# Kernel tuning notes

Hardware: AMD Instinct MI355X
Metric: run time of the kernel (lower is better)

Reference implementation:

```python
import jax, jax.numpy as jnp
import numpy as np

EPS = 1e-8

def _gelu(x):
    return jax.nn.gelu(x, approximate=False)  # torch F.gelu default (erf)

def _film_pool(feat, q, film_w, film_b, hid_w, hid_b, fin_w, fin_b):
    # feat: (B,C,H,W), q: (B,Q,E)
    B, C, H, W = feat.shape
    f = feat.reshape(B, C, H * W).transpose(0, 2, 1)            # (B,HW,C)
    gb = q @ film_w + film_b                                    # (B,Q,2C)
    gamma, beta = jnp.split(gb, 2, axis=-1)                     # (B,Q,C) each
    mod = gamma[:, :, None, :] * f[:, None, :, :] + beta[:, :, None, :]  # (B,Q,HW,C)
    h = _gelu(mod @ hid_w + hid_b)                              # (B,Q,HW,Hh)
    attn = jax.nn.sigmoid(h @ fin_w + fin_b)                    # (B,Q,HW,1)
    pooled = (attn * mod).sum(axis=2) / (attn.sum(axis=2) + EPS)  # (B,Q,C)
    return pooled, attn[..., 0]                                 # attn map (B,Q,HW)

def setup_inputs() -> dict:
    key = jax.random.key(0)
    ks = jax.random.split(key, 32)
    B, Q, E, Hh = 2, 32, 768, 128
    chans = [64, 128, 256]
    hws = [(80, 80), (40, 40), (20, 20)]
    d = {}
    d['feat0'] = jax.random.normal(ks[0], (B, chans[0], *hws[0]), jnp.float32)
    d['feat1'] = jax.random.normal(ks[1], (B, chans[1], *hws[1]), jnp.float32)
    d['feat2'] = jax.random.normal(ks[2], (B, chans[2], *hws[2]), jnp.float32)
    d['fact_embeddings'] = jax.random.normal(ks[3], (B, Q, E), jnp.float32)
    for i, C in enumerate(chans):
        d[f'film_w{i}'] = jax.random.normal(ks[4 + 4 * i], (E, 2 * C), jnp.float32) * 0.02
        d[f'film_b{i}'] = jnp.zeros((2 * C,), jnp.float32)
        d[f'hid_w{i}'] = jax.random.normal(ks[5 + 4 * i], (C, Hh), jnp.float32) * 0.05
        d[f'hid_b{i}'] = jnp.zeros((Hh,), jnp.float32)
        d[f'fin_w{i}'] = jax.random.normal(ks[6 + 4 * i], (Hh, 1), jnp.float32) * 0.05
        d[f'fin_b{i}'] = jnp.zeros((1,), jnp.float32)
    in_dim = sum(chans) + hws[-1][0] * hws[-1][1]  # 448 + 400 = 848
    d['mlp_w1'] = jax.random.normal(ks[20], (in_dim, 512), jnp.float32) * 0.02
    d['mlp_b1'] = jnp.zeros((512,), jnp.float32)
    d['mlp_w2'] = jax.random.normal(ks[21], (512, 256), jnp.float32) * 0.02
    d['mlp_b2'] = jnp.zeros((256,), jnp.float32)
    d['mlp_w3'] = jax.random.normal(ks[22], (256, 1), jnp.float32) * 0.02
    d['mlp_b3'] = jnp.zeros((1,), jnp.float32)
    return d

def reference(feat0, feat1, feat2, fact_embeddings,
              film_w0, film_b0, hid_w0, hid_b0, fin_w0, fin_b0,
              film_w1, film_b1, hid_w1, hid_b1, fin_w1, fin_b1,
              film_w2, film_b2, hid_w2, hid_b2, fin_w2, fin_b2,
              mlp_w1, mlp_b1, mlp_w2, mlp_b2, mlp_w3, mlp_b3):
    q = fact_embeddings
    p0, _ = _film_pool(feat0, q, film_w0, film_b0, hid_w0, hid_b0, fin_w0, fin_b0)
    p1, _ = _film_pool(feat1, q, film_w1, film_b1, hid_w1, hid_b1, fin_w1, fin_b1)
    p2, a2 = _film_pool(feat2, q, film_w2, film_b2, hid_w2, hid_b2, fin_w2, fin_b2)
    cat = jnp.concatenate([p0, p1, p2, a2], axis=2)  # (B,Q,848)
    x = _gelu(cat @ mlp_w1 + mlp_b1)
    x = _gelu(x @ mlp_w2 + mlp_b2)
    logits = (x @ mlp_w3 + mlp_b3)[..., 0]  # (B,Q)
    return logits
```

## Files before the change

kernel.cpp:

```cpp
#include <hip/hip_runtime.h>
#include <math.h>

#define BQ 64
#define HH 128
#define EPS 1e-8f

typedef short bf16x8 __attribute__((ext_vector_type(8)));
typedef float f32x4  __attribute__((ext_vector_type(4)));

__device__ __forceinline__ float gelu_exact(float x) {
    return 0.5f * x * (1.0f + erff(x * 0.70710678118654752440f));
}

__device__ __forceinline__ unsigned bf16_rne(float x) {
    unsigned u = __float_as_uint(x);
    return (u + 0x7FFFu + ((u >> 16) & 1u)) >> 16;
}
__device__ __forceinline__ uint2 split_pack(float a, float b) {
    unsigned ha = bf16_rne(a);
    float fa = __uint_as_float(ha << 16);
    unsigned la = bf16_rne(a - fa);
    unsigned hb = bf16_rne(b);
    float fb = __uint_as_float(hb << 16);
    unsigned lb = bf16_rne(b - fb);
    uint2 r; r.x = ha | (hb << 16); r.y = la | (lb << 16);
    return r;
}

__device__ __forceinline__
void pack_feat_body(int i,
                    const float* __restrict__ f0, const float* __restrict__ f1,
                    const float* __restrict__ f2,
                    unsigned short* __restrict__ p0h, unsigned short* __restrict__ p0l,
                    unsigned short* __restrict__ p1h, unsigned short* __restrict__ p1l,
                    unsigned short* __restrict__ p2h, unsigned short* __restrict__ p2l)
{
    const float* f; unsigned short *oh, *ol; int HW; int idx;
    if (i < 102400)      { f = f0; oh = p0h; ol = p0l; HW = 6400; idx = i; }
    else if (i < 153600) { f = f1; oh = p1h; ol = p1l; HW = 1600; idx = i - 102400; }
    else if (i < 179200) { f = f2; oh = p2h; ol = p2l; HW = 400;  idx = i - 153600; }
    else return;
    const int px = idx % HW;
    const int cgb = idx / HW;
    const float* src = f + ((size_t)cgb * 8) * HW + px;
    float a[8];
    #pragma unroll
    for (int k = 0; k < 8; ++k) a[k] = src[(size_t)k * HW];
    unsigned hwd[4], lwd[4];
    #pragma unroll
    for (int k = 0; k < 4; ++k) {
        uint2 p = split_pack(a[2 * k], a[2 * k + 1]);
        hwd[k] = p.x; lwd[k] = p.y;
    }
    *(uint4*)&oh[(size_t)idx * 8] = make_uint4(hwd[0], hwd[1], hwd[2], hwd[3]);
    *(uint4*)&ol[(size_t)idx * 8] = make_uint4(lwd[0], lwd[1], lwd[2], lwd[3]);
}

__global__ __launch_bounds__(256)
void prep1_kernel(const float* __restrict__ f0, const float* __restrict__ f1,
                  const float* __restrict__ f2,
                  unsigned short* __restrict__ p0h, unsigned short* __restrict__ p0l,
                  unsigned short* __restrict__ p1h, unsigned short* __restrict__ p1l,
                  unsigned short* __restrict__ p2h, unsigned short* __restrict__ p2l,
                  const float* __restrict__ qe,
                  const float* __restrict__ fw0, const float* __restrict__ fb0,
                  const float* __restrict__ fw1, const float* __restrict__ fb1,
                  const float* __restrict__ fw2, const float* __restrict__ fb2,
                  float* __restrict__ gb0, float* __restrict__ gb1, float* __restrict__ gb2)
{
    const int tid = threadIdx.x;
    if (blockIdx.x < 700) {
        pack_feat_body(blockIdx.x * 256 + tid, f0, f1, f2, p0h, p0l, p1h, p1l, p2h, p2l);
        return;
    }
    __shared__ float sq[768];
    __shared__ float sP[256];
    const int bb = blockIdx.x - 700;
    const int chunk = bb >> 6, bq = bb & 63;
    int s, o0;
    if (chunk == 0)      { s = 0; o0 = 0; }
    else if (chunk <= 2) { s = 1; o0 = (chunk - 1) * 128; }
    else                 { s = 2; o0 = (chunk - 3) * 128; }
    const float* fw  = s == 0 ? fw0 : s == 1 ? fw1 : fw2;
    const float* fbv = s == 0 ? fb0 : s == 1 ? fb1 : fb2;
    float* gb        = s == 0 ? gb0 : s == 1 ? gb1 : gb2;
    const int twoC = 128 << s;

    for (int i = tid; i < 768; i += 256) sq[i] = qe[bq * 768 + i];
    __syncthreads();
    const int o = o0 + (tid & 127), half = tid >> 7;
    const int e0 = half * 384;
    float a0 = 0.f, a1 = 0.f;
    #pragma unroll 2
    for (int e = 0; e < 384; e += 2) {
        a0 = fmaf(sq[e0 + e],     fw[(e0 + e) * twoC + o],     a0);
        a1 = fmaf(sq[e0 + e + 1], fw[(e0 + e + 1) * twoC + o], a1);
    }
    sP[tid] = a0 + a1;
    __syncthreads();
    if (tid < 128) {
        int oo = o0 + tid;
        gb[bq * twoC + oo] = sP[tid] + sP[tid + 128] + fbv[oo];
    }
}

__global__ __launch_bounds__(256)
void prep2_kernel(const float* __restrict__ gb0, const float* __restrict__ gb1,
                  const float* __restrict__ gb2,
                  const float* __restrict__ hw0_, const float* __restrict__ hb0,
                  const float* __restrict__ hw1_, const float* __restrict__ hb1,
                  const float* __restrict__ hw2_, const float* __restrict__ hb2,
                  unsigned short* __restrict__ g0h, unsigned short* __restrict__ g0l,
                  unsigned short* __restrict__ g1h, unsigned short* __restrict__ g1l,
                  unsigned short* __restrict__ g2h, unsigned short* __restrict__ g2l,
                  float* __restrict__ b20, float* __restrict__ b21, float* __restrict__ b22)
{
    const int tid = threadIdx.x;
    if (blockIdx.x < 1792) {
        int i = blockIdx.x * 256 + tid;
        const float *gb, *hw; unsigned short *oh, *ol; int C, idx;
        if (i < 65536)       { gb = gb0; hw = hw0_; oh = g0h; ol = g0l; C = 64;  idx = i; }
        else if (i < 196608) { gb = gb1; hw = hw1_; oh = g1h; ol = g1l; C = 128; idx = i - 65536; }
        else                 { gb = gb2; hw = hw2_; oh = g2h; ol = g2l; C = 256; idx = i - 196608; }
        const int j  = idx & 127;
        const int cg = (idx >> 7) % (C / 8);
        const int bq = idx / (128 * (C / 8));
        const int c0 = cg * 8;
        const float* g = gb + bq * 2 * C;
        float a[8];
        #pragma unroll
        for (int k = 0; k < 8; ++k) a[k] = g[c0 + k] * hw[(size_t)(c0 + k) * HH + j];
        unsigned hwd[4], lwd[4];
        #pragma unroll
        for (int k = 0; k < 4; ++k) {
            uint2 p = split_pack(a[2 * k], a[2 * k + 1]);
            hwd[k] = p.x; lwd[k] = p.y;
        }
        *(uint4*)&oh[(size_t)idx * 8] = make_uint4(hwd[0], hwd[1], hwd[2], hwd[3]);
        *(uint4*)&ol[(size_t)idx * 8] = make_uint4(lwd[0], lwd[1], lwd[2], lwd[3]);
        return;
    }
    __shared__ float sBeta[256];
    __shared__ float sP[256];
    const int bb = blockIdx.x - 1792;
    const int s = bb >> 6, bq = bb & 63;
    const float* gb = s == 0 ? gb0 : s == 1 ? gb1 : gb2;
    const float* hw = s == 0 ? hw0_ : s == 1 ? hw1_ : hw2_;
    const float* hb = s == 0 ? hb0 : s == 1 ? hb1 : hb2;
    float* b2       = s == 0 ? b20 : s == 1 ? b21 : b22;
    const int C = 64 << s;

    for (int i = tid; i < C; i += 256) sBeta[i] = gb[bq * 2 * C + C + i];
    __syncthreads();
    const int j = tid & 127, half = tid >> 7;
    const int c0 = half * (C / 2);
    float acc = 0.f;
    for (int c = 0; c < C / 2; ++c)
        acc = fmaf(sBeta[c0 + c], hw[(c0 + c) * HH + j], acc);
    sP[tid] = acc;
    __syncthreads();
    if (tid < 128) b2[bq * HH + tid] = hb[tid] + sP[tid] + sP[tid + 128];
}

#define MFMA3(ACC, ALO, AHI, BH, BL)                                            \
    ACC = __builtin_amdgcn_mfma_f32_16x16x32_bf16(ALO, BH, ACC, 0, 0, 0);       \
    ACC = __builtin_amdgcn_mfma_f32_16x16x32_bf16(AHI, BL, ACC, 0, 0, 0);       \
    ACC = __builtin_amdgcn_mfma_f32_16x16x32_bf16(AHI, BH, ACC, 0, 0, 0);

template<int C, bool WRITE_ATTN>
__device__ __forceinline__
void pool_body(const float* __restrict__ feat, int HW,
               const unsigned short* __restrict__ fh, const unsigned short* __restrict__ fl,
               const unsigned short* __restrict__ gwh, const unsigned short* __restrict__ gwl,
               const float* __restrict__ b2, const float* __restrict__ finw,
               const float* __restrict__ finb,
               float* __restrict__ Sout, float* __restrict__ attn_out,
               int b, int qp, int tile,
               unsigned short* sB, float* sAttn)
{
    const int tid  = threadIdx.x;
    const int w    = tid >> 6;
    const int lane = tid & 63;
    const int l15  = lane & 15, l4 = lane >> 4;
    const int px0  = tile * 256;
    constexpr int CG = C / 8;
    const int bq0 = b * 32 + qp * 2;
    const int bq1 = bq0 + 1;
    const float* fbase = feat + (size_t)b * C * HW;

    f32x4 accA[2][8], accB[2][8];
    #pragma unroll
    for (int jt = 0; jt < 8; ++jt) {
        float bv0 = b2[bq0 * HH + jt * 16 + l15];
        float bv1 = b2[bq1 * HH + jt * 16 + l15];
        accA[0][jt] = (f32x4){bv0, bv0, bv0, bv0};
        accA[1][jt] = (f32x4){bv0, bv0, bv0, bv0};
        accB[0][jt] = (f32x4){bv1, bv1, bv1, bv1};
        accB[1][jt] = (f32x4){bv1, bv1, bv1, bv1};
    }

    const int apx0 = min(px0 + (w * 2 + 0) * 16 + l15, HW - 1);
    const int apx1 = min(px0 + (w * 2 + 1) * 16 + l15, HW - 1);
    const unsigned short* fhp = fh + (size_t)b * CG * HW * 8;
    const unsigned short* flp = fl + (size_t)b * CG * HW * 8;
    const unsigned short* q0h = gwh + (size_t)bq0 * CG * 1024;
    const unsigned short* q0l = gwl + (size_t)bq0 * CG * 1024;
    const unsigned short* q1h = gwh + (size_t)bq1 * CG * 1024;
    const unsigned short* q1l = gwl + (size_t)bq1 * CG * 1024;

    for (int ks = 0; ks < CG / 4; ++ks) {
        const size_t arow = (size_t)(ks * 4 + l4) * HW;
        const bf16x8 Ahi0 = *(const bf16x8*)(fhp + (arow + apx0) * 8);
        const bf16x8 Alo0 = *(const bf16x8*)(flp + (arow + apx0) * 8);
        const bf16x8 Ahi1 = *(const bf16x8*)(fhp + (arow + apx1) * 8);
        const bf16x8 Alo1 = *(const bf16x8*)(flp + (arow + apx1) * 8);
        {
            uint4* dst = (uint4*)sB;
            dst[tid]        = ((const uint4*)(q0h + (size_t)ks * 4096))[tid];
            dst[512  + tid] = ((const uint4*)(q0l + (size_t)ks * 4096))[tid];
            dst[1024 + tid] = ((const uint4*)(q1h + (size_t)ks * 4096))[tid];
            dst[1536 + tid] = ((const uint4*)(q1l + (size_t)ks * 4096))[tid];
        }
        __syncthreads();
        const int bofs = (l4 * 128 + l15) * 8;
        #pragma unroll
        for (int jt = 0; jt < 8; ++jt) {
            const bf16x8 B0h = *(const bf16x8*)(sB + bofs + jt * 128);
            const bf16x8 B0l = *(const bf16x8*)(sB + 4096 + bofs + jt * 128);
            MFMA3(accA[0][jt], Alo0, Ahi0, B0h, B0l)
            MFMA3(accA[1][jt], Alo1, Ahi1, B0h, B0l)
            const bf16x8 B1h = *(const bf16x8*)(sB + 8192 + bofs + jt * 128);
            const bf16x8 B1l = *(const bf16x8*)(sB + 12288 + bofs + jt * 128);
            MFMA3(accB[0][jt], Alo0, Ahi0, B1h, B1l)
            MFMA3(accB[1][jt], Alo1, Ahi1, B1h, B1l)
        }
        __syncthreads();
    }

    const float fb0 = finb[0];
    #pragma unroll
    for (int pt = 0; pt < 2; ++pt) {
        float p0[4] = {0.f, 0.f, 0.f, 0.f};
        float p1[4] = {0.f, 0.f, 0.f, 0.f};
        #pragma unroll
        for (int jt = 0; jt < 8; ++jt) {
            float fwv = finw[jt * 16 + l15];
            #pragma unroll
            for (int r = 0; r < 4; ++r) {
                p0[r] = fmaf(gelu_exact(accA[pt][jt][r]), fwv, p0[r]);
                p1[r] = fmaf(gelu_exact(accB[pt][jt][r]), fwv, p1[r]);
            }
        }
        #pragma unroll
        for (int r = 0; r < 4; ++r) {
            p0[r] += __shfl_xor(p0[r], 1);  p1[r] += __shfl_xor(p1[r], 1);
            p0[r] += __shfl_xor(p0[r], 2);  p1[r] += __shfl_xor(p1[r], 2);
            p0[r] += __shfl_xor(p0[r], 4);  p1[r] += __shfl_xor(p1[r], 4);
            p0[r] += __shfl_xor(p0[r], 8);  p1[r] += __shfl_xor(p1[r], 8);
        }
        if (l15 == 0) {
            #pragma unroll
            for (int r = 0; r < 4; ++r) {
                int lpx = (w * 2 + pt) * 16 + l4 * 4 + r;
                int px  = px0 + lpx;
                float a0v = (px < HW) ? 1.0f / (1.0f + expf(-(p0[r] + fb0))) : 0.0f;
                float a1v = (px < HW) ? 1.0f / (1.0f + expf(-(p1[r] + fb0))) : 0.0f;
                sAttn[lpx]       = a0v;
                sAttn[256 + lpx] = a1v;
                if (WRITE_ATTN && px < HW) {
                    attn_out[bq0 * HW + px] = a0v;
                    attn_out[bq1 * HW + px] = a1v;
                }
            }
        }
    }
    __syncthreads();

    {
        float sa = sAttn[tid];
        #pragma unroll
        for (int d = 1; d < 64; d <<= 1) sa += __shfl_xor(sa, d);
        if (lane == 0) {
            int bqx = (tid < 256) ? bq0 : bq1;
            atomicAdd(&Sout[bqx * (C + 1) + C], sa);
        }
    }

    constexpr int CPW = C / 8;
    #pragma unroll 1
    for (int ci = 0; ci < CPW; ++ci) {
        const int c2 = w * CPW + ci;
        const float* fr = fbase + (size_t)c2 * HW;
        float s0 = 0.f, s1 = 0.f;
        #pragma unroll
        for (int k = 0; k < 4; ++k) {
            int lpx = lane + 64 * k;
            int gc = min(px0 + lpx, HW - 1);
            float fv = fr[gc];
            s0 = fmaf(fv, sAttn[lpx], s0);
            s1 = fmaf(fv, sAttn[256 + lpx], s1);
        }
        #pragma unroll
        for (int d = 1; d < 64; d <<= 1) {
            s0 += __shfl_xor(s0, d);
            s1 += __shfl_xor(s1, d);
        }
        if (lane == 0) {
            atomicAdd(&Sout[bq0 * (C + 1) + c2], s0);
            atomicAdd(&Sout[bq1 * (C + 1) + c2], s1);
        }
    }
}

__global__ __launch_bounds__(512)
void pool_fused(const unsigned short* __restrict__ f0h, const unsigned short* __restrict__ f0l,
                const unsigned short* __restrict__ f1h, const unsigned short* __restrict__ f1l,
                const unsigned short* __restrict__ f2h, const unsigned short* __restrict__ f2l,
                const unsigned short* __restrict__ g0h, const unsigned short* __restrict__ g0l,
                const unsigned short* __restrict__ g1h, const unsigned short* __restrict__ g1l,
                const unsigned short* __restrict__ g2h, const unsigned short* __restrict__ g2l,
                const float* __restrict__ feat0, const float* __restrict__ feat1,
                const float* __restrict__ feat2,
                const float* __restrict__ b20, const float* __restrict__ b21,
                const float* __restrict__ b22,
                const float* __restrict__ finw0, const float* __restrict__ finb0,
                const float* __restrict__ finw1, const float* __restrict__ finb1,
                const float* __restrict__ finw2, const float* __restrict__ finb2,
                float* __restrict__ S0, float* __restrict__ S1, float* __restrict__ S2,
                float* __restrict__ attn2)
{
    __shared__ __align__(16) unsigned short sB[16384];
    __shared__ float sAttn[512];
    const int blk = blockIdx.x;
    if (blk < 64) {
        int bt = blk >> 4, qp = blk & 15;
        int b = bt >> 1, t = bt & 1;
        pool_body<256, true>(feat2, 400, f2h, f2l, g2h, g2l, b22, finw2, finb2,
                             S2, attn2, b, qp, t, sB, sAttn);
    } else if (blk < 288) {
        int bb = blk - 64; int bt = bb >> 4, qp = bb & 15;
        int b = bt / 7, t = bt % 7;
        pool_body<128, false>(feat1, 1600, f1h, f1l, g1h, g1l, b21, finw1, finb1,
                              S1, nullptr, b, qp, t, sB, sAttn);
    } else {
        int bb = blk - 288; int bt = bb >> 4, qp = bb & 15;
        int b = bt / 25, t = bt % 25;
        pool_body<64, false>(feat0, 6400, f0h, f0l, g0h, g0l, b20, finw0, finb0,
                             S0, nullptr, b, qp, t, sB, sAttn);
    }
}

__global__ __launch_bounds__(256)
void mlp1_kernel(const float* __restrict__ S0, const float* __restrict__ S1,
                 const float* __restrict__ S2,
                 const float* __restrict__ gb0, const float* __restrict__ gb1,
                 const float* __restrict__ gb2,
                 const float* __restrict__ attn2,
                 const float* __restrict__ w1, const float* __restrict__ b1,
                 float* __restrict__ X1)
{
    __shared__ float sCat[848];
    __shared__ float sP[256];
    const int tid = threadIdx.x, bq = blockIdx.x;

    for (int i = tid; i < 448; i += 256) {
        int sc, c;
        if (i < 64)       { sc = 0; c = i; }
        else if (i < 192) { sc = 1; c = i - 64; }
        else              { sc = 2; c = i - 192; }
        const int C = 64 << sc;
        const float* So = (sc == 0) ? S0 : (sc == 1) ? S1 : S2;
        const float* g  = (sc == 0) ? gb0 : (sc == 1) ? gb1 : gb2;
        float Sa = So[bq * (C + 1) + C];
        float Sf = So[bq * (C + 1) + c];
        float gamma = g[bq * 2 * C + c];
        float beta  = g[bq * 2 * C + C + c];
        sCat[i] = (gamma * Sf + beta * Sa) / (Sa + EPS);
    }
    for (int i = tid; i < 400; i += 256) sCat[448 + i] = attn2[bq * 400 + i];
    __syncthreads();

    const int o = blockIdx.y * 128 + (tid & 127), half = tid >> 7;
    const int k0 = half * 424;
    float a0 = 0.f, a1 = 0.f;
    #pragma unroll 2
    for (int k = 0; k < 424; k += 2) {
        a0 = fmaf(sCat[k0 + k],     w1[(k0 + k) * 512 + o],     a0);
        a1 = fmaf(sCat[k0 + k + 1], w1[(k0 + k + 1) * 512 + o], a1);
    }
    sP[tid] = a0 + a1;
    __syncthreads();
    if (tid < 128) {
        int oo = blockIdx.y * 128 + tid;
        X1[bq * 512 + oo] = sP[tid] + sP[tid + 128] + b1[oo];
    }
}

__global__ __launch_bounds__(256)
void mlp23_kernel(const float* __restrict__ X1,
                  const float* __restrict__ w2, const float* __restrict__ b2,
                  const float* __restrict__ w3, const float* __restrict__ b3,
                  float* __restrict__ out)
{
    __shared__ float sX1[512];
    __shared__ float sX2[256];
    __shared__ float sR[4];
    const int tid = threadIdx.x, bq = blockIdx.x;
    for (int i = tid; i < 512; i += 256) sX1[i] = gelu_exact(X1[bq * 512 + i]);
    __syncthreads();
    float a0 = b2[tid], a1 = 0.f, a2 = 0.f, a3 = 0.f;
    #pragma unroll 4
    for (int k = 0; k < 512; k += 4) {
        a0 = fmaf(sX1[k],     w2[(k)     * 256 + tid], a0);
        a1 = fmaf(sX1[k + 1], w2[(k + 1) * 256 + tid], a1);
        a2 = fmaf(sX1[k + 2], w2[(k + 2) * 256 + tid], a2);
        a3 = fmaf(sX1[k + 3], w2[(k + 3) * 256 + tid], a3);
    }
    sX2[tid] = gelu_exact((a0 + a1) + (a2 + a3));
    __syncthreads();
    float p = sX2[tid] * w3[tid];
    #pragma unroll
    for (int d = 1; d < 64; d <<= 1) p += __shfl_xor(p, d);
    if ((tid & 63) == 0) sR[tid >> 6] = p;
    __syncthreads();
    if (tid == 0) out[bq] = sR[0] + sR[1] + sR[2] + sR[3] + b3[0];
}

extern "C" void kernel_launch(void* const* d_in, const int* in_sizes, int n_in,
                              void* d_out, int out_size, void* d_ws, size_t ws_size,
                              hipStream_t stream)
{
    const float* feat0 = (const float*)d_in[0];
    const float* feat1 = (const float*)d_in[1];
    const float* feat2 = (const float*)d_in[2];
    const float* qe    = (const float*)d_in[3];
    const float* film_w0 = (const float*)d_in[4];
    const float* film_b0 = (const float*)d_in[5];
    const float* hid_w0  = (const float*)d_in[6];
    const float* hid_b0  = (const float*)d_in[7];
    const float* fin_w0  = (const float*)d_in[8];
    const float* fin_b0  = (const float*)d_in[9];
    const float* film_w1 = (const float*)d_in[10];
    const float* film_b1 = (const float*)d_in[11];
    const float* hid_w1  = (const float*)d_in[12];
    const float* hid_b1  = (const float*)d_in[13];
    const float* fin_w1  = (const float*)d_in[14];
    const float* fin_b1  = (const float*)d_in[15];
    const float* film_w2 = (const float*)d_in[16];
    const float* film_b2 = (const float*)d_in[17];
    const float* hid_w2  = (const float*)d_in[18];
    const float* hid_b2  = (const float*)d_in[19];
    const float* fin_w2  = (const float*)d_in[20];
    const float* fin_b2  = (const float*)d_in[21];
    const float* mlp_w1  = (const float*)d_in[22];
    const float* mlp_b1  = (const float*)d_in[23];
    const float* mlp_w2  = (const float*)d_in[24];
    const float* mlp_b2  = (const float*)d_in[25];
    const float* mlp_w3  = (const float*)d_in[26];
    const float* mlp_b3  = (const float*)d_in[27];

    float* ws = (float*)d_ws;
    float* S0    = ws;
    float* S1    = ws + 4160;
    float* S2    = ws + 12416;
    float* gb0   = ws + 28864;
    float* gb1   = ws + 37056;
    float* gb2   = ws + 53440;
    float* b20   = ws + 86208;
    float* b21   = ws + 94400;
    float* b22   = ws + 102592;
    float* attn2 = ws + 110784;
    float* X1    = ws + 136384;

    unsigned short* us = (unsigned short*)(ws + 169216);
    unsigned short* f0h = us;
    unsigned short* f0l = f0h + 819200;
    unsigned short* f1h = f0l + 819200;
    unsigned short* f1l = f1h + 409600;
    unsigned short* f2h = f1l + 409600;
    unsigned short* f2l = f2h + 204800;
    unsigned short* g0h = f2l + 204800;
    unsigned short* g0l = g0h + 524288;
    unsigned short* g1h = g0l + 524288;
    unsigned short* g1l = g1h + 1048576;
    unsigned short* g2h = g1l + 1048576;
    unsigned short* g2l = g2h + 2097152;

    hipMemsetAsync(d_ws, 0, 28864 * sizeof(float), stream);

    prep1_kernel<<<1148, 256, 0, stream>>>(
        feat0, feat1, feat2, f0h, f0l, f1h, f1l, f2h, f2l,
        qe, film_w0, film_b0, film_w1, film_b1, film_w2, film_b2,
        gb0, gb1, gb2);

    prep2_kernel<<<1984, 256, 0, stream>>>(
        gb0, gb1, gb2,
        hid_w0, hid_b0, hid_w1, hid_b1, hid_w2, hid_b2,
        g0h, g0l, g1h, g1l, g2h, g2l,
        b20, b21, b22);

    pool_fused<<<1088, 512, 0, stream>>>(
        f0h, f0l, f1h, f1l, f2h, f2l,
        g0h, g0l, g1h, g1l, g2h, g2l,
        feat0, feat1, feat2,
        b20, b21, b22,
        fin_w0, fin_b0, fin_w1, fin_b1, fin_w2, fin_b2,
        S0, S1, S2, attn2);

    mlp1_kernel<<<dim3(BQ, 4), 256, 0, stream>>>(
        S0, S1, S2, gb0, gb1, gb2, attn2, mlp_w1, mlp_b1, X1);

    mlp23_kernel<<<BQ, 256, 0, stream>>>(
        X1, mlp_w2, mlp_b2, mlp_w3, mlp_b3, (float*)d_out);
}
```

Baseline: 235.3 us.

## Rebalance pool kernel into persistent-style blocks processing multiple tiles

```diff
diff --git a/kernel.cpp b/kernel.cpp
--- a/kernel.cpp
+++ b/kernel.cpp
@@ -310,6 +310,7 @@
             atomicAdd(&Sout[bq1 * (C + 1) + c2], s1);
         }
     }
+    __syncthreads();
 }
 
 __global__ __launch_bounds__(512)
@@ -332,22 +333,35 @@
     __shared__ __align__(16) unsigned short sB[16384];
     __shared__ float sAttn[512];
     const int blk = blockIdx.x;
+
+    #define RUN_S2(IDX) {                                                        \
+        int qp = (IDX) & 15, r = (IDX) >> 4;                                     \
+        pool_body<256, true>(feat2, 400, f2h, f2l, g2h, g2l, b22, finw2, finb2,  \
+                             S2, attn2, r >> 1, qp, r & 1, sB, sAttn); }
+    #define RUN_S1(IDX) {                                                        \
+        int qp = (IDX) & 15, bt = (IDX) >> 4;                                    \
+        pool_body<128, false>(feat1, 1600, f1h, f1l, g1h, g1l, b21, finw1, finb1,\
+                              S1, nullptr, bt / 7, qp, bt % 7, sB, sAttn); }
+    #define RUN_S0(IDX) {                                                        \
+        int qp = (IDX) & 15, bt = (IDX) >> 4;                                    \
+        pool_body<64, false>(feat0, 6400, f0h, f0l, g0h, g0l, b20, finw0, finb0, \
+                             S0, nullptr, bt / 25, qp, bt % 25, sB, sAttn); }
+
     if (blk < 64) {
-        int bt = blk >> 4, qp = blk & 15;
-        int b = bt >> 1, t = bt & 1;
-        pool_body<256, true>(feat2, 400, f2h, f2l, g2h, g2l, b22, finw2, finb2,
-                             S2, attn2, b, qp, t, sB, sAttn);
+        RUN_S2(blk)
     } else if (blk < 288) {
-        int bb = blk - 64; int bt = bb >> 4, qp = bb & 15;
-        int b = bt / 7, t = bt % 7;
-        pool_body<128, false>(feat1, 1600, f1h, f1l, g1h, g1l, b21, finw1, finb1,
-                              S1, nullptr, b, qp, t, sB, sAttn);
+        int j = blk - 64;
+        RUN_S1(j)
+        RUN_S0(j)
     } else {
-        int bb = blk - 288; int bt = bb >> 4, qp = bb & 15;
-        int b = bt / 25, t = bt % 25;
-        pool_body<64, false>(feat0, 6400, f0h, f0l, g0h, g0l, b20, finw0, finb0,
-                             S0, nullptr, b, qp, t, sB, sAttn);
-    }
+        int j = blk - 288;
+        RUN_S0(224 + j)
+        RUN_S0(448 + j)
+        if (j < 128) RUN_S0(672 + j)
+    }
+    #undef RUN_S2
+    #undef RUN_S1
+    #undef RUN_S0
 }
 
 __global__ __launch_bounds__(256)
@@ -499,7 +513,7 @@
         g0h, g0l, g1h, g1l, g2h, g2l,
         b20, b21, b22);
 
-    pool_fused<<<1088, 512, 0, stream>>>(
+    pool_fused<<<512, 512, 0, stream>>>(
         f0h, f0l, f1h, f1l, f2h, f2l,
         g0h, g0l, g1h, g1l, g2h, g2l,
         feat0, feat1, feat2,
```

Result: slower. 252.3 us (+7.2%).
